# Performance work log

Measured on AMD Instinct MI355X. Metric: run time of the kernel, lower is better.

The kernel has to match this reference:

```python
import jax, jax.numpy as jnp
import numpy as np

B, S, IN, H, BB, M = 256, 512, 64, 256, 256, 64


def _lecun_tanh(x):
    return 1.7159 * jnp.tanh(0.666 * x)


def setup_inputs() -> dict:
    key = jax.random.key(0)
    ks = jax.random.split(key, 32)
    def g(i, shape, fan_in):
        return jax.random.normal(ks[i], shape, jnp.float32) * (fan_in ** -0.5)
    return {
        "x": jax.random.normal(ks[0], (B, S, IN), jnp.float32),
        "timespans": jax.random.uniform(ks[1], (B, S), jnp.float32, minval=0.01, maxval=1.0),
        "hx": jnp.zeros((B, H), jnp.float32),
        # CfC cell backbone (2 layers, lecun_tanh)
        "bb_w0": g(2, (IN + H, BB), IN + H), "bb_b0": jnp.zeros((BB,), jnp.float32),
        "bb_w1": g(3, (BB, BB), BB), "bb_b1": jnp.zeros((BB,), jnp.float32),
        # CfC heads ff1/ff2/time_a/time_b
        "ff1_w": g(4, (BB, H), BB), "ff1_b": jnp.zeros((H,), jnp.float32),
        "ff2_w": g(5, (BB, H), BB), "ff2_b": jnp.zeros((H,), jnp.float32),
        "ta_w": g(6, (BB, H), BB), "ta_b": jnp.zeros((H,), jnp.float32),
        "tb_w": g(7, (BB, H), BB), "tb_b": jnp.zeros((H,), jnp.float32),
        # projection hidden -> motor
        "proj_w": g(8, (H, M), H), "proj_b": jnp.zeros((M,), jnp.float32),
        # intensity head: M->16 SiLU ->3 Softplus
        "ih_w0": g(9, (M, 16), M), "ih_b0": jnp.zeros((16,), jnp.float32),
        "ih_w1": g(10, (16, 3), 16), "ih_b1": jnp.zeros((3,), jnp.float32),
        # action head: M->16 SiLU ->1 Tanh
        "ah_w0": g(11, (M, 16), M), "ah_b0": jnp.zeros((16,), jnp.float32),
        "ah_w1": g(12, (16, 1), 16), "ah_b1": jnp.zeros((1,), jnp.float32),
        # confidence head: M->8 SiLU ->1 Sigmoid
        "ch_w0": g(13, (M, 8), M), "ch_b0": jnp.zeros((8,), jnp.float32),
        "ch_w1": g(14, (8, 1), 8), "ch_b1": jnp.zeros((1,), jnp.float32),
    }


def reference(x, timespans, hx, bb_w0, bb_b0, bb_w1, bb_b1, ff1_w, ff1_b, ff2_w, ff2_b,
              ta_w, ta_b, tb_w, tb_b, proj_w, proj_b,
              ih_w0, ih_b0, ih_w1, ih_b1, ah_w0, ah_b0, ah_w1, ah_b1,
              ch_w0, ch_b0, ch_w1, ch_b1):
    ts = timespans[..., None]  # (B,S,1)

    def step(h, inp):
        x_t, ts_t = inp  # (B,IN), (B,1)
        z = jnp.concatenate([x_t, h], axis=-1)
        z = _lecun_tanh(z @ bb_w0 + bb_b0)
        z = _lecun_tanh(z @ bb_w1 + bb_b1)
        ff1 = jnp.tanh(z @ ff1_w + ff1_b)
        ff2 = jnp.tanh(z @ ff2_w + ff2_b)
        t_interp = jax.nn.sigmoid((z @ ta_w + ta_b) * ts_t + (z @ tb_w + tb_b))
        h_new = ff1 * (1.0 - t_interp) + t_interp * ff2
        return h_new, h_new

    xs = (jnp.swapaxes(x, 0, 1), jnp.swapaxes(ts, 0, 1))  # time-major
    h_n, h_seq = jax.lax.scan(step, hx, xs)               # h_seq: (S,B,H)
    cfc = jnp.swapaxes(h_seq, 0, 1) @ proj_w + proj_b     # (B,S,M)
    intensities = jax.nn.softplus(jax.nn.silu(cfc @ ih_w0 + ih_b0) @ ih_w1 + ih_b1)
    actions = jnp.tanh(jax.nn.silu(cfc @ ah_w0 + ah_b0) @ ah_w1 + ah_b1)
    confidence = jax.nn.sigmoid(jax.nn.silu(cfc @ ch_w0 + ch_b0) @ ch_w1 + ch_b1)
    return intensities, actions, confidence, h_n
```

## Files before the change

### kernel.cpp

```cpp
#include <hip/hip_runtime.h>
#include <hip/hip_bf16.h>

#define BN  256
#define SN  512
#define INN 64
#define HN  256
#define MN  64

#define ZINS 328
#define ZBS  264
#define CFS  72
#define HTS  36

#define OFF_ACT  393216
#define OFF_CONF 524288
#define OFF_HN   655360

#define FLAG_STRIDE 32
#define FLAG_BYTES  16384

typedef _Float16 h8 __attribute__((ext_vector_type(8)));
typedef float fx4 __attribute__((ext_vector_type(4)));
typedef unsigned long long u64;

union h4u {
    _Float16 h[4];
    u64 u;
};

__device__ __forceinline__ fx4 mfma16(h8 a, h8 b, fx4 c) {
    return __builtin_amdgcn_mfma_f32_16x16x32_f16(a, b, c, 0, 0, 0);
}
__device__ __forceinline__ float fast_tanh(float x) {
    float e = __expf(2.0f * x);
    return 1.0f - 2.0f / (e + 1.0f);
}
__device__ __forceinline__ float fast_sig(float x) { return 1.0f / (1.0f + __expf(-x)); }
__device__ __forceinline__ float lecun_tanh(float x) { return 1.7159f * fast_tanh(0.666f * x); }
__device__ __forceinline__ float softplus_f(float x) {
    return fmaxf(x, 0.0f) + __logf(1.0f + __expf(-fabsf(x)));
}

template <int NW>
__device__ __forceinline__ h8 loadB(const float* __restrict__ w, int col, int kbase) {
    h8 r;
#pragma unroll
    for (int j = 0; j < 8; ++j) r[j] = (_Float16)w[(kbase + j) * NW + col];
    return r;
}

__global__ void __launch_bounds__(512, 1) lh_scan_kernel(
    const float* __restrict__ x, const float* __restrict__ tsp, const float* __restrict__ hx,
    const float* __restrict__ w0, const float* __restrict__ b0,
    const float* __restrict__ w1, const float* __restrict__ b1,
    const float* __restrict__ f1w, const float* __restrict__ f1b,
    const float* __restrict__ f2w, const float* __restrict__ f2b,
    const float* __restrict__ taw, const float* __restrict__ tab,
    const float* __restrict__ tbw, const float* __restrict__ tbb,
    const float* __restrict__ pw, const float* __restrict__ pbias,
    const float* __restrict__ ihw0, const float* __restrict__ ihb0,
    const float* __restrict__ ihw1, const float* __restrict__ ihb1,
    const float* __restrict__ ahw0, const float* __restrict__ ahb0,
    const float* __restrict__ ahw1, const float* __restrict__ ahb1,
    const float* __restrict__ chw0, const float* __restrict__ chb0,
    const float* __restrict__ chw1, const float* __restrict__ chb1,
    float* __restrict__ out, unsigned int* __restrict__ flags,
    u64* __restrict__ hbuf)
{
    __shared__ __align__(16) _Float16 zin[16 * ZINS];
    __shared__ __align__(16) _Float16 z0b[16 * ZBS];
    __shared__ __align__(16) _Float16 z1b[16 * ZBS];
    __shared__ __align__(16) _Float16 cfcb[16 * CFS];
    __shared__ __align__(16) _Float16 pfl[8 * 4 * 64 * 8];
    __shared__ __align__(16) _Float16 w1l[8 * 8 * 64 * 8];
    __shared__ __align__(16) float htmp[4 * 16 * HTS];
    __shared__ float hidI[16 * 16];
    __shared__ float hidA[16 * 16];
    __shared__ float hidC[16 * 8];
    __shared__ float tsb[2][16];
    __shared__ float wsm[80];

    const int tid  = threadIdx.x;
    const int wv   = tid >> 6;
    const int lane = tid & 63;
    const int lo   = lane & 15;
    const int hi   = lane >> 4;
    const int hi8  = hi * 8;

    const int bid   = blockIdx.x;
    const int xcd   = bid & 7;
    const int c     = (bid >> 3) & 7;
    const int gsel  = bid >> 6;
    const int g     = xcd + 8 * gsel;
    const int bg    = g * 16;
    const int sbase = c * 32;

    if (tid < 48)          wsm[tid] = ihw1[tid];
    else if (tid < 51)     wsm[tid] = ihb1[tid - 48];
    else if (tid < 67)     wsm[tid] = ahw1[tid - 51];
    else if (tid == 67)    wsm[67]  = ahb1[0];
    else if (tid < 76)     wsm[tid] = chw1[tid - 68];
    else if (tid == 76)    wsm[76]  = chb1[0];

    {
        int r = tid >> 5, c8 = (tid & 31) * 8;
#pragma unroll
        for (int j = 0; j < 8; ++j)
            zin[r * ZINS + 64 + c8 + j] = (_Float16)hx[(bg + r) * HN + c8 + j];
        int c2 = (tid & 31) * 2;
        const float* xp = &x[((size_t)(bg + r) * SN + 0) * INN + c2];
        zin[r * ZINS + c2]     = (_Float16)xp[0];
        zin[r * ZINS + c2 + 1] = (_Float16)xp[1];
    }
    if (tid < 16) tsb[0][tid] = tsp[(bg + tid) * SN + 0];

    const int cg0 = wv, cg1 = wv + 8;
    const float b00 = b0[cg0 * 16 + lo], b01 = b0[cg1 * 16 + lo];
    const float b10 = b1[cg0 * 16 + lo], b11 = b1[cg1 * 16 + lo];

    const int hm  = wv >> 1;
    const int hcol = sbase + (wv & 1) * 16 + lo;
    const float* hwp = (hm == 0) ? f1w : (hm == 1) ? f2w : (hm == 2) ? taw : tbw;
    const float* hbp = (hm == 0) ? f1b : (hm == 1) ? f2b : (hm == 2) ? tab : tbb;
    const float hb = hbp[hcol];

    h8 w0f0[10], w0f1[10], w1f0[8], hdf[8];
#pragma unroll
    for (int kk = 0; kk < 10; ++kk) {
        w0f0[kk] = loadB<256>(w0, cg0 * 16 + lo, kk * 32 + hi8);
        w0f1[kk] = loadB<256>(w0, cg1 * 16 + lo, kk * 32 + hi8);
    }
#pragma unroll
    for (int kk = 0; kk < 8; ++kk) {
        w1f0[kk] = loadB<256>(w1, cg0 * 16 + lo, kk * 32 + hi8);
        hdf[kk]  = loadB<256>(hwp, hcol, kk * 32 + hi8);
        h8 f = loadB<256>(w1, cg1 * 16 + lo, kk * 32 + hi8);
        *(h8*)&w1l[((kk * 8 + wv) * 64 + lane) * 8] = f;
    }
    float pbv = 0.0f;
    if (wv < 4) {
        pbv = pbias[wv * 16 + lo];
#pragma unroll
        for (int kk = 0; kk < 8; ++kk) {
            h8 f = loadB<64>(pw, wv * 16 + lo, kk * 32 + hi8);
            *(h8*)&pfl[((kk * 4 + wv) * 64 + lane) * 8] = f;
        }
    }
    h8 hwf[2] = {};
    float hbv = 0.0f;
    if (wv == 4) {
        hbv = ihb0[lo];
#pragma unroll
        for (int kk = 0; kk < 2; ++kk) hwf[kk] = loadB<16>(ihw0, lo, kk * 32 + hi8);
    } else if (wv == 5) {
        hbv = ahb0[lo];
#pragma unroll
        for (int kk = 0; kk < 2; ++kk) hwf[kk] = loadB<16>(ahw0, lo, kk * 32 + hi8);
    } else if (wv == 6) {
        int cc = (lo < 8) ? lo : 0;
        hbv = (lo < 8) ? chb0[lo] : 0.0f;
#pragma unroll
        for (int kk = 0; kk < 2; ++kk) hwf[kk] = loadB<8>(chw0, cc, kk * 32 + hi8);
    }

    __syncthreads();

    for (int t = 0; t <= SN; ++t) {
        const int pr = t & 7;

        if (t < SN) {
            fx4 a0 = {b00, b00, b00, b00}, a1 = {b01, b01, b01, b01};
#pragma unroll
            for (int kk = 0; kk < 10; ++kk) {
                h8 a = *(const h8*)&zin[lo * ZINS + kk * 32 + hi8];
                a0 = mfma16(a, w0f0[kk], a0);
                a1 = mfma16(a, w0f1[kk], a1);
            }
#pragma unroll
            for (int i = 0; i < 4; ++i) {
                int r = hi * 4 + i;
                z0b[r * ZBS + cg0 * 16 + lo] = (_Float16)lecun_tanh(a0[i]);
                z0b[r * ZBS + cg1 * 16 + lo] = (_Float16)lecun_tanh(a1[i]);
            }
        }
        __syncthreads();

        if (t + 1 < SN) {
            int r = tid >> 5, c2 = (tid & 31) * 2;
            const float* xp = &x[((size_t)(bg + r) * SN + (t + 1)) * INN + c2];
            zin[r * ZINS + c2]     = (_Float16)xp[0];
            zin[r * ZINS + c2 + 1] = (_Float16)xp[1];
            if (tid < 16) tsb[(t + 1) & 1][tid] = tsp[(bg + tid) * SN + t + 1];
        }

        if (t < SN) {
            fx4 a0 = {b10, b10, b10, b10}, a1 = {b11, b11, b11, b11};
#pragma unroll
            for (int kk = 0; kk < 8; ++kk) {
                h8 a = *(const h8*)&z0b[lo * ZBS + kk * 32 + hi8];
                h8 b1f = *(const h8*)&w1l[((kk * 8 + wv) * 64 + lane) * 8];
                a0 = mfma16(a, w1f0[kk], a0);
                a1 = mfma16(a, b1f, a1);
            }
#pragma unroll
            for (int i = 0; i < 4; ++i) {
                int r = hi * 4 + i;
                z1b[r * ZBS + cg0 * 16 + lo] = (_Float16)lecun_tanh(a0[i]);
                z1b[r * ZBS + cg1 * 16 + lo] = (_Float16)lecun_tanh(a1[i]);
            }
        }
        __syncthreads();

        if (t < SN) {
            fx4 acc = {hb, hb, hb, hb};
#pragma unroll
            for (int kk = 0; kk < 8; ++kk) {
                h8 a = *(const h8*)&z1b[lo * ZBS + kk * 32 + hi8];
                acc = mfma16(a, hdf[kk], acc);
            }
#pragma unroll
            for (int i = 0; i < 4; ++i)
                htmp[(hm * 16 + hi * 4 + i) * HTS + (wv & 1) * 16 + lo] = acc[i];
        }
        __syncthreads();

        if (t < SN && tid < 128) {
            int r = tid >> 3, c4 = (tid & 7) * 4;
            h4u pk;
            float hn3 = 0.0f;
#pragma unroll
            for (int k = 0; k < 4; ++k) {
                float a1v = htmp[(0 * 16 + r) * HTS + c4 + k];
                float a2v = htmp[(1 * 16 + r) * HTS + c4 + k];
                float a3v = htmp[(2 * 16 + r) * HTS + c4 + k];
                float a4v = htmp[(3 * 16 + r) * HTS + c4 + k];
                float tv  = tsb[t & 1][r];
                float ff1 = fast_tanh(a1v);
                float ff2 = fast_tanh(a2v);
                float ti  = fast_sig(a3v * tv + a4v);
                float hn  = ff1 + ti * (ff2 - ff1);
                pk.h[k] = (_Float16)hn;
                if (t == SN - 1) out[OFF_HN + (bg + r) * HN + sbase + c4 + k] = hn;
                hn3 = hn;
            }
            (void)hn3;
            size_t idx = ((((size_t)((t + 1) & 1) * 16 + g) * 16) + r) * 64 + (sbase + c4) / 4;
            __hip_atomic_store(&hbuf[idx], pk.u, __ATOMIC_RELAXED, __HIP_MEMORY_SCOPE_AGENT);
        }
        __syncthreads();
        if (t < SN && tid == 0)
            __hip_atomic_store(&flags[(g * 8 + c) * FLAG_STRIDE], (unsigned)(t + 1),
                               __ATOMIC_RELAXED, __HIP_MEMORY_SCOPE_AGENT);

        if (t >= 1 && c == pr && wv < 4) {
            fx4 acc = {pbv, pbv, pbv, pbv};
#pragma unroll
            for (int kk = 0; kk < 8; ++kk) {
                h8 a = *(const h8*)&zin[lo * ZINS + 64 + kk * 32 + hi8];
                h8 b = *(const h8*)&pfl[((kk * 4 + wv) * 64 + lane) * 8];
                acc = mfma16(a, b, acc);
            }
#pragma unroll
            for (int i = 0; i < 4; ++i)
                cfcb[(hi * 4 + i) * CFS + wv * 16 + lo] = (_Float16)acc[i];
        }
        __syncthreads();

        if (t >= 1 && c == pr && wv >= 4 && wv < 7) {
            fx4 acc = {hbv, hbv, hbv, hbv};
#pragma unroll
            for (int kk = 0; kk < 2; ++kk) {
                h8 a = *(const h8*)&cfcb[lo * CFS + kk * 32 + hi8];
                acc = mfma16(a, hwf[kk], acc);
            }
#pragma unroll
            for (int i = 0; i < 4; ++i) {
                float v = acc[i];
                v = v * fast_sig(v);
                int r = hi * 4 + i;
                if (wv == 4)       hidI[r * 16 + lo] = v;
                else if (wv == 5)  hidA[r * 16 + lo] = v;
                else if (lo < 8)   hidC[r * 8 + lo]  = v;
            }
        }
        __syncthreads();

        if (t >= 1 && c == pr && tid < 80) {
            int r = tid / 5, o = tid % 5;
            int tc = t - 1;
            int b = bg + r;
            if (o < 3) {
                float s = wsm[48 + o];
#pragma unroll
                for (int u = 0; u < 16; ++u) s += hidI[r * 16 + u] * wsm[u * 3 + o];
                out[(size_t)(b * SN + tc) * 3 + o] = softplus_f(s);
            } else if (o == 3) {
                float s = wsm[67];
#pragma unroll
                for (int u = 0; u < 16; ++u) s += hidA[r * 16 + u] * wsm[51 + u];
                out[OFF_ACT + b * SN + tc] = fast_tanh(s);
            } else {
                float s = wsm[76];
#pragma unroll
                for (int u = 0; u < 8; ++u) s += hidC[r * 8 + u] * wsm[68 + u];
                out[OFF_CONF + b * SN + tc] = fast_sig(s);
            }
        }

        if (t < SN) {
            if (tid < 8) {
                unsigned target = (unsigned)(t + 1);
                while (__hip_atomic_load(&flags[(g * 8 + tid) * FLAG_STRIDE],
                                         __ATOMIC_RELAXED, __HIP_MEMORY_SCOPE_AGENT) < target) {}
            }
            __syncthreads();
            {
                int r = tid >> 5, c8 = (tid & 31) * 8;
                size_t idx = ((((size_t)((t + 1) & 1) * 16 + g) * 16) + r) * 64 + c8 / 4;
                u64 v0 = __hip_atomic_load(&hbuf[idx],     __ATOMIC_RELAXED, __HIP_MEMORY_SCOPE_AGENT);
                u64 v1 = __hip_atomic_load(&hbuf[idx + 1], __ATOMIC_RELAXED, __HIP_MEMORY_SCOPE_AGENT);
                *(u64*)&zin[r * ZINS + 64 + c8]     = v0;
                *(u64*)&zin[r * ZINS + 64 + c8 + 4] = v1;
            }
        }
        __syncthreads();
    }
}

extern "C" void kernel_launch(void* const* d_in, const int* in_sizes, int n_in,
                              void* d_out, int out_size, void* d_ws, size_t ws_size,
                              hipStream_t stream) {
    (void)in_sizes; (void)n_in; (void)out_size; (void)ws_size;
    const float* p[29];
    for (int i = 0; i < 29; ++i) p[i] = (const float*)d_in[i];
    unsigned int* flags = (unsigned int*)d_ws;
    u64* hbuf = (u64*)((char*)d_ws + FLAG_BYTES);
    hipMemsetAsync(d_ws, 0, FLAG_BYTES, stream);
    hipLaunchKernelGGL(lh_scan_kernel, dim3(128), dim3(512), 0, stream,
        p[0], p[1], p[2], p[3], p[4], p[5], p[6], p[7], p[8], p[9], p[10], p[11], p[12],
        p[13], p[14], p[15], p[16], p[17], p[18], p[19], p[20], p[21], p[22], p[23],
        p[24], p[25], p[26], p[27], p[28], (float*)d_out, flags, hbuf);
}
```

Measured before the change: 2.325 ms.

## Replace flag-based cross-block sync with tag bits embedded in hidden-state data

Drops the per-block progress flags and the spin-then-barrier-then-load handshake. Each published fp16 hidden value now carries a 2-bit step tag in the mantissa LSBs of two halves per 64-bit word, so consumers spin directly on the data words until the tag matches. This removes a flag store, a flag poll round-trip and one __syncthreads per step from the critical recurrence path. In exchange it loses one mantissa bit on some hidden values, relies on 64-bit atomic store granularity, and needs an 0xAA memset for initial tags.

```diff
diff --git a/kernel.cpp b/kernel.cpp
--- a/kernel.cpp
+++ b/kernel.cpp
@@ -16,17 +16,13 @@
 #define OFF_CONF 524288
 #define OFF_HN   655360
 
-#define FLAG_STRIDE 32
-#define FLAG_BYTES  16384
+#define HBUF_OFF 16384
+#define HBUF_BYTES (2 * 256 * 64 * 8)
 
 typedef _Float16 h8 __attribute__((ext_vector_type(8)));
 typedef float fx4 __attribute__((ext_vector_type(4)));
 typedef unsigned long long u64;
-
-union h4u {
-    _Float16 h[4];
-    u64 u;
-};
+union h4u { _Float16 h[4]; unsigned short s[4]; u64 u; };
 
 __device__ __forceinline__ fx4 mfma16(h8 a, h8 b, fx4 c) {
     return __builtin_amdgcn_mfma_f32_16x16x32_f16(a, b, c, 0, 0, 0);
@@ -64,8 +60,7 @@
     const float* __restrict__ ahw1, const float* __restrict__ ahb1,
     const float* __restrict__ chw0, const float* __restrict__ chb0,
     const float* __restrict__ chw1, const float* __restrict__ chb1,
-    float* __restrict__ out, unsigned int* __restrict__ flags,
-    u64* __restrict__ hbuf)
+    float* __restrict__ out, u64* __restrict__ hbuf)
 {
     __shared__ __align__(16) _Float16 zin[16 * ZINS];
     __shared__ __align__(16) _Float16 z0b[16 * ZBS];
@@ -118,7 +113,7 @@
     const float b00 = b0[cg0 * 16 + lo], b01 = b0[cg1 * 16 + lo];
     const float b10 = b1[cg0 * 16 + lo], b11 = b1[cg1 * 16 + lo];
 
-    const int hm  = wv >> 1;
+    const int hm   = wv >> 1;
     const int hcol = sbase + (wv & 1) * 16 + lo;
     const float* hwp = (hm == 0) ? f1w : (hm == 1) ? f2w : (hm == 2) ? taw : tbw;
     const float* hbp = (hm == 0) ? f1b : (hm == 1) ? f2b : (hm == 2) ? tab : tbb;
@@ -167,6 +162,7 @@
 
     for (int t = 0; t <= SN; ++t) {
         const int pr = t & 7;
+        const unsigned tagc = ((((unsigned)(t + 1)) >> 1) + 1u) & 3u;
 
         if (t < SN) {
             fx4 a0 = {b00, b00, b00, b00}, a1 = {b01, b01, b01, b01};
@@ -198,9 +194,9 @@
 #pragma unroll
             for (int kk = 0; kk < 8; ++kk) {
                 h8 a = *(const h8*)&z0b[lo * ZBS + kk * 32 + hi8];
-                h8 b1f = *(const h8*)&w1l[((kk * 8 + wv) * 64 + lane) * 8];
+                h8 bf = *(const h8*)&w1l[((kk * 8 + wv) * 64 + lane) * 8];
                 a0 = mfma16(a, w1f0[kk], a0);
-                a1 = mfma16(a, b1f, a1);
+                a1 = mfma16(a, bf, a1);
             }
 #pragma unroll
             for (int i = 0; i < 4; ++i) {
@@ -227,30 +223,26 @@
         if (t < SN && tid < 128) {
             int r = tid >> 3, c4 = (tid & 7) * 4;
             h4u pk;
-            float hn3 = 0.0f;
+            float tv = tsb[t & 1][r];
 #pragma unroll
             for (int k = 0; k < 4; ++k) {
                 float a1v = htmp[(0 * 16 + r) * HTS + c4 + k];
                 float a2v = htmp[(1 * 16 + r) * HTS + c4 + k];
                 float a3v = htmp[(2 * 16 + r) * HTS + c4 + k];
                 float a4v = htmp[(3 * 16 + r) * HTS + c4 + k];
-                float tv  = tsb[t & 1][r];
                 float ff1 = fast_tanh(a1v);
                 float ff2 = fast_tanh(a2v);
                 float ti  = fast_sig(a3v * tv + a4v);
                 float hn  = ff1 + ti * (ff2 - ff1);
                 pk.h[k] = (_Float16)hn;
+                unsigned tb = (k & 1) ? ((tagc >> 1) & 1u) : (tagc & 1u);
+                pk.s[k] = (unsigned short)((pk.s[k] & 0xFFFEu) | tb);
                 if (t == SN - 1) out[OFF_HN + (bg + r) * HN + sbase + c4 + k] = hn;
-                hn3 = hn;
-            }
-            (void)hn3;
-            size_t idx = ((((size_t)((t + 1) & 1) * 16 + g) * 16) + r) * 64 + (sbase + c4) / 4;
+            }
+            size_t idx = (((size_t)((t + 1) & 1) * 256) + g * 16 + r) * 64 + (sbase + c4) / 4;
             __hip_atomic_store(&hbuf[idx], pk.u, __ATOMIC_RELAXED, __HIP_MEMORY_SCOPE_AGENT);
         }
         __syncthreads();
-        if (t < SN && tid == 0)
-            __hip_atomic_store(&flags[(g * 8 + c) * FLAG_STRIDE], (unsigned)(t + 1),
-                               __ATOMIC_RELAXED, __HIP_MEMORY_SCOPE_AGENT);
 
         if (t >= 1 && c == pr && wv < 4) {
             fx4 acc = {pbv, pbv, pbv, pbv};
@@ -308,20 +300,17 @@
         }
 
         if (t < SN) {
-            if (tid < 8) {
-                unsigned target = (unsigned)(t + 1);
-                while (__hip_atomic_load(&flags[(g * 8 + tid) * FLAG_STRIDE],
-                                         __ATOMIC_RELAXED, __HIP_MEMORY_SCOPE_AGENT) < target) {}
-            }
-            __syncthreads();
-            {
-                int r = tid >> 5, c8 = (tid & 31) * 8;
-                size_t idx = ((((size_t)((t + 1) & 1) * 16 + g) * 16) + r) * 64 + c8 / 4;
-                u64 v0 = __hip_atomic_load(&hbuf[idx],     __ATOMIC_RELAXED, __HIP_MEMORY_SCOPE_AGENT);
-                u64 v1 = __hip_atomic_load(&hbuf[idx + 1], __ATOMIC_RELAXED, __HIP_MEMORY_SCOPE_AGENT);
-                *(u64*)&zin[r * ZINS + 64 + c8]     = v0;
-                *(u64*)&zin[r * ZINS + 64 + c8 + 4] = v1;
-            }
+            int r = tid >> 5, c8 = (tid & 31) * 8;
+            size_t idx = (((size_t)((t + 1) & 1) * 256) + g * 16 + r) * 64 + c8 / 4;
+            const unsigned b0e = tagc & 1u, b1e = (tagc >> 1) & 1u;
+            u64 v0 = __hip_atomic_load(&hbuf[idx],     __ATOMIC_RELAXED, __HIP_MEMORY_SCOPE_AGENT);
+            u64 v1 = __hip_atomic_load(&hbuf[idx + 1], __ATOMIC_RELAXED, __HIP_MEMORY_SCOPE_AGENT);
+            while ((unsigned)(v0 & 1u) != b0e || (unsigned)((v0 >> 16) & 1u) != b1e)
+                v0 = __hip_atomic_load(&hbuf[idx],     __ATOMIC_RELAXED, __HIP_MEMORY_SCOPE_AGENT);
+            while ((unsigned)(v1 & 1u) != b0e || (unsigned)((v1 >> 16) & 1u) != b1e)
+                v1 = __hip_atomic_load(&hbuf[idx + 1], __ATOMIC_RELAXED, __HIP_MEMORY_SCOPE_AGENT);
+            *(u64*)&zin[r * ZINS + 64 + c8]     = v0;
+            *(u64*)&zin[r * ZINS + 64 + c8 + 4] = v1;
         }
         __syncthreads();
     }
@@ -333,11 +322,10 @@
     (void)in_sizes; (void)n_in; (void)out_size; (void)ws_size;
     const float* p[29];
     for (int i = 0; i < 29; ++i) p[i] = (const float*)d_in[i];
-    unsigned int* flags = (unsigned int*)d_ws;
-    u64* hbuf = (u64*)((char*)d_ws + FLAG_BYTES);
-    hipMemsetAsync(d_ws, 0, FLAG_BYTES, stream);
+    u64* hbuf = (u64*)((char*)d_ws + HBUF_OFF);
+    hipMemsetAsync(hbuf, 0xAA, HBUF_BYTES, stream);
     hipLaunchKernelGGL(lh_scan_kernel, dim3(128), dim3(512), 0, stream,
         p[0], p[1], p[2], p[3], p[4], p[5], p[6], p[7], p[8], p[9], p[10], p[11], p[12],
         p[13], p[14], p[15], p[16], p[17], p[18], p[19], p[20], p[21], p[22], p[23],
-        p[24], p[25], p[26], p[27], p[28], (float*)d_out, flags, hbuf);
-}
+        p[24], p[25], p[26], p[27], p[28], (float*)d_out, hbuf);
+}
```

New measurement: 2.390 ms. 1.03x slower.
